# Performance work log

Hardware: AMD Instinct MI355X
Metric: run time of the kernel (lower is better)

The kernel has to match this reference:

```python
import jax, jax.numpy as jnp
import numpy as np

B, N, E, F, H, L = 64, 1024, 32768, 128, 32, 2
K = N // 2          # topk ratio 0.5 (fixed in source forward)
NB = 5              # num_neighbors: point cloud points per node
CF, P = 5, 50       # PI channels (filtration methods), PI_dim
OUT = 2

def gcn_conv(x, src, dst, emask, W, b, n):
    # PyG GCNConv: project first, symmetric norm with self-loops; emask zeroes filtered edges
    h = x @ W
    deg = jax.ops.segment_sum(emask, dst, num_segments=n) + 1.0
    dinv = jax.lax.rsqrt(deg)
    coef = (dinv[src] * dinv[dst] * emask)[:, None]
    agg = jax.ops.segment_sum(h[src] * coef, dst, num_segments=n)
    return agg + h * (dinv * dinv)[:, None] + b

def tcl(t, A, Bf, C):
    # Tensor Contraction Layer: mode-1/2/3 factor contraction
    return jnp.einsum('bijk,pi,qj,rk->bpqr', t, A, Bf, C)

def mlp2(h, Wa, ba, Wb, bb):
    return jax.nn.relu(h @ Wa + ba) @ Wb + bb

def setup_inputs():
    key = jax.random.key(0)
    ks = jax.random.split(key, 32)
    s = 0.05
    return {
        'x1': jax.random.normal(ks[0], (B, N, F), jnp.float32),
        'edge_index1': jax.random.randint(ks[1], (B, 2, E), 0, N),
        'PI1': jax.random.uniform(ks[2], (B, CF, P, P), dtype=jnp.float32),
        'x2': jax.random.normal(ks[3], (B, N, F), jnp.float32),
        'edge_index2': jax.random.randint(ks[4], (B, 2, E), 0, N),
        'PI2': jax.random.uniform(ks[5], (B, CF, P, P), dtype=jnp.float32),
        'W_score': jax.random.normal(ks[6], (F, NB * 2)) * s,
        'b_score': jnp.zeros((NB * 2,)),
        'W_gcn0': jax.random.normal(ks[7], (F, H)) * s,
        'b_gcn0': jnp.zeros((H,)),
        'Wm0a': jax.random.normal(ks[8], (H, H)) * s,
        'bm0a': jnp.zeros((H,)),
        'Wm0b': jax.random.normal(ks[9], (H, H * H)) * s,
        'bm0b': jnp.zeros((H * H,)),
        'W_gcn1': jax.random.normal(ks[10], (H * H, H)) * s,
        'b_gcn1': jnp.zeros((H,)),
        'Wm1a': jax.random.normal(ks[11], (H, H)) * s,
        'bm1a': jnp.zeros((H,)),
        'Wm1b': jax.random.normal(ks[12], (H, H * H)) * s,
        'bm1b': jnp.zeros((H * H,)),
        'F0': jax.random.normal(ks[13], (H, L)) * s,
        'F1': jax.random.normal(ks[14], (H, H)) * s,
        'F2': jax.random.normal(ks[15], (H, H)) * s,
        'K_conv': jax.random.normal(ks[16], (H, CF, 2, 2)) * s,
        'b_conv': jnp.zeros((H,)),
        'G0': jax.random.normal(ks[17], (H, H)) * s,
        'G1': jax.random.normal(ks[18], (H, P // 2)) * s,
        'G2': jax.random.normal(ks[19], (H, P // 2)) * s,
        'H0': jax.random.normal(ks[20], (2 * H, 2 * H)) * s,
        'H1': jax.random.normal(ks[21], (H, H)) * s,
        'H2': jax.random.normal(ks[22], (H, H)) * s,
        'Wo1': jax.random.normal(ks[23], (H, H)) * s,
        'bo1': jnp.zeros((H,)),
        'Wo2': jax.random.normal(ks[24], (H, OUT)) * s,
        'bo2': jnp.zeros((OUT,)),
    }

def reference(x1, edge_index1, PI1, x2, edge_index2, PI2, W_score, b_score,
              W_gcn0, b_gcn0, Wm0a, bm0a, Wm0b, bm0b,
              W_gcn1, b_gcn1, Wm1a, bm1a, Wm1b, bm1b,
              F0, F1, F2, K_conv, b_conv, G0, G1, G2,
              H0, H1, H2, Wo1, bo1, Wo2, bo2):
    ones = jnp.ones((E,), jnp.float32)

    def pool_one(xg, s_, d_):
        # score_node_layer -> point cloud -> lifespan score -> topk(0.5) -> filter_adj
        emb = gcn_conv(xg, s_, d_, ones, W_score, b_score, N)
        pc = emb.reshape(N, NB, 2)
        score = jnp.abs(pc[..., 1] - pc[..., 0]).sum(-1)
        _, perm = jax.lax.top_k(score, K)
        newidx = jnp.full((N,), -1).at[perm].set(jnp.arange(K))
        r, c = newidx[s_], newidx[d_]
        valid = (r >= 0) & (c >= 0)
        return xg[perm], jnp.where(valid, r, 0), jnp.where(valid, c, 0), valid.astype(jnp.float32)

    def branch(x, ei, PI):
        src, dst = ei[:, 0, :], ei[:, 1, :]
        xp, psrc, pdst, em = jax.vmap(pool_one)(x, src, dst)
        conv0 = jax.vmap(lambda h, s_, d_, m: gcn_conv(h, s_, d_, m, W_gcn0, b_gcn0, K))
        conv1 = jax.vmap(lambda h, s_, d_, m: gcn_conv(h, s_, d_, m, W_gcn1, b_gcn1, K))
        h1 = mlp2(conv0(xp, psrc, pdst, em), Wm0a, bm0a, Wm0b, bm0b)   # [B,K,H*H]
        h2 = mlp2(conv1(h1, psrc, pdst, em), Wm1a, bm1a, Wm1b, bm1b)   # [B,K,H*H]
        g = jnp.stack([h1.mean(1), h2.mean(1)], axis=1).reshape(B, L, H, H)
        gcn_t = tcl(g, F0, F1, F2)                                      # [B,H,H,H]
        pe = jax.lax.conv_general_dilated(PI, K_conv, (2, 2), 'VALID',
                                          dimension_numbers=('NCHW', 'OIHW', 'NCHW'))
        pe = jax.nn.relu(pe + b_conv[None, :, None, None])              # [B,H,25,25]
        pi_t = tcl(pe, G0, G1, G2)                                      # [B,H,H,H]
        fused = tcl(jnp.concatenate([gcn_t, pi_t], axis=1), H0, H1, H2) # [B,2H,H,H]
        pooled = fused.mean(axis=(1, 3))                                # [B,H]
        return jax.nn.relu(pooled @ Wo1 + bo1) @ Wo2 + bo2              # [B,OUT]

    return jnp.stack([branch(x1, edge_index1, PI1), branch(x2, edge_index2, PI2)])
```

## Files before the change

### kernel.cpp

```cpp
#include <hip/hip_runtime.h>
#include <cstdint>


constexpr int B_ = 64, N_ = 1024, E_ = 32768, F_ = 128, H_ = 32;
constexpr int CF_ = 5, P_ = 50, K_ = 512, G_ = 128, PO = 25;

constexpr size_t WS_SRCS  = 0;
constexpr size_t WS_ONODE = WS_SRCS + (size_t)G_*(E_/2);
constexpr size_t WS_VDEG  = WS_ONODE + (size_t)G_*K_;
constexpr size_t WS_EOFF  = WS_VDEG + (size_t)G_*(K_/2);
constexpr size_t WS_DINV  = WS_EOFF + (size_t)G_*K_;
constexpr size_t WS_GA    = WS_DINV + (size_t)G_*K_;
constexpr size_t WS_GC    = WS_GA + (size_t)G_*K_*H_;
constexpr size_t WS_PM0   = WS_GC + (size_t)G_*K_*H_;
constexpr size_t WS_PM1   = WS_PM0 + (size_t)G_*64;
constexpr size_t WS_PPI   = WS_PM1 + (size_t)G_*64;
constexpr size_t WS_F0V   = WS_PPI + (size_t)G_*32;
constexpr size_t WS_B01   = WS_F0V + 32;
constexpr size_t WS_C0B   = WS_B01 + 32;
constexpr size_t WS_C1B   = WS_C0B + 32;
constexpr size_t WS_W01   = WS_C1B + 32;
constexpr size_t WS_P0B   = WS_W01 + 1024;
constexpr size_t WS_P1B   = WS_P0B + 1024;

constexpr size_t WS_DSC   = WS_GC;

static __device__ __forceinline__ int swzf4(int row, int c4) {
  return row*32 + (((c4) ^ ((row >> 2) & 7)) << 2);
}

__global__ __launch_bounds__(512, 4) void kA_pre(
    const float* __restrict__ x1, const float* __restrict__ x2,
    const float* __restrict__ Wsc,
    const float* __restrict__ F0w, const float* __restrict__ F2w,
    const float* __restrict__ H0w, const float* __restrict__ H2w,
    const float* __restrict__ Wm0b, const float* __restrict__ bm0b,
    const float* __restrict__ Wm1b, const float* __restrict__ bm1b,
    const float* __restrict__ Wg1, float* __restrict__ ws)
{
  __shared__ float SM[640];
  int blk = blockIdx.x, t = threadIdx.x;

  if (blk < 8*G_) {
    int g = blk >> 3, sub = blk & 7, br = g >> 6, b = g & 63;
    const float* xg = (br ? x2 : x1) + (size_t)b*N_*F_;
    float* WdL = SM;
    if (t < F_) {
      #pragma unroll
      for (int j = 0; j < 5; ++j) WdL[t*5+j] = Wsc[t*10+2*j+1] - Wsc[t*10+2*j];
    }
    __syncthreads();
    int row = sub*128 + (t >> 2), q = t & 3;
    const float4* xr = (const float4*)(xg + (size_t)row*F_);
    float acc[5] = {};
    #pragma unroll
    for (int i = 0; i < 8; ++i) {
      int k4 = q + 4*i;
      float4 v = xr[k4];
      const float* w = &WdL[k4*20];
      #pragma unroll
      for (int j = 0; j < 5; ++j)
        acc[j] += v.x*w[j] + v.y*w[5+j] + v.z*w[10+j] + v.w*w[15+j];
    }
    #pragma unroll
    for (int j = 0; j < 5; ++j) {
      acc[j] += __shfl_xor(acc[j], 1, 4);
      acc[j] += __shfl_xor(acc[j], 2, 4);
    }
    if (q == 0) {
      float* o = ws + WS_DSC + ((size_t)g*N_ + row)*5;
      #pragma unroll
      for (int j = 0; j < 5; ++j) o[j] = acc[j];
    }
    return;
  }

  int blk2 = blk - 8*G_;
  if (blk2 == 0) {
    float* h0mS = SM;
    if (t < 32) { float s = 0.f; for (int qq = 0; qq < 64; ++qq) s += H0w[qq*64+t]; h0mS[t] = s*(1.f/64.f); }
    __syncthreads();
    if (t < 2) { float s = 0.f; for (int p = 0; p < 32; ++p) s += F0w[p*2+t]*h0mS[p]; ws[WS_F0V+t] = s; }
  } else if (blk2 <= 32) {
    int kk = blk2 - 1;
    int ol = t >> 4, seg = t & 15;
    const float4* ar = (const float4*)(Wm0b + (size_t)kk*1024 + seg*64);
    float s = 0.f;
    #pragma unroll
    for (int i = 0; i < 16; ++i) {
      float4 a = ar[i];
      int tt = seg*64 + i*4;
      s += a.x*Wg1[(tt+0)*32 + ol] + a.y*Wg1[(tt+1)*32 + ol]
         + a.z*Wg1[(tt+2)*32 + ol] + a.w*Wg1[(tt+3)*32 + ol];
    }
    s += __shfl_xor(s, 1, 16);
    s += __shfl_xor(s, 2, 16);
    s += __shfl_xor(s, 4, 16);
    s += __shfl_xor(s, 8, 16);
    if (seg == 0) ws[WS_W01 + kk*32 + ol] = s;
  } else if (blk2 == 33) {
    float* red = SM;
    int j = t & 31, seg = t >> 5;
    float s = 0.f;
    #pragma unroll
    for (int i = 0; i < 64; ++i) {
      int k = seg*64 + i;
      s += bm0b[k]*Wg1[k*32 + j];
    }
    red[seg*32 + j] = s;
    __syncthreads();
    if (t < 32) {
      float a = 0.f;
      #pragma unroll
      for (int q = 0; q < 16; ++q) a += red[q*32 + t];
      ws[WS_B01 + t] = a;
    }
  } else {
    const float* Wb = (blk2 == 34) ? Wm0b : Wm1b;
    const float* bb = (blk2 == 34) ? bm0b : bm1b;
    size_t dstP = (blk2 == 34) ? WS_P0B : WS_P1B;
    size_t dstC = (blk2 == 34) ? WS_C0B : WS_C1B;
    float* h2mL = SM;
    float* f2vL = SM + 32;
    if (t < 32) { float s = 0.f; for (int r = 0; r < 32; ++r) s += H2w[r*32+t]; h2mL[t] = s*(1.f/32.f); }
    __syncthreads();
    if (t < 32) { float s = 0.f; for (int r = 0; r < 32; ++r) s += F2w[r*32+t]*h2mL[r]; f2vL[t] = s; }
    __syncthreads();
    if (t < 256) {
      #pragma unroll
      for (int q = 0; q < 4; ++q) {
        int e = t*4 + q;
        int k = e >> 5, c = e & 31;
        float s = 0.f;
        #pragma unroll
        for (int kp = 0; kp < 32; ++kp) s += Wb[k*1024 + c*32 + kp]*f2vL[kp];
        ws[dstP + e] = s;
      }
    }
    if (t < 32) {
      float s = 0.f;
      #pragma unroll
      for (int kp = 0; kp < 32; ++kp) s += bb[t*32+kp]*f2vL[kp];
      ws[dstC+t] = s;
    }
  }
}

__global__ __launch_bounds__(256, 4) void kPI(
    const float* __restrict__ PI1, const float* __restrict__ PI2,
    const float* __restrict__ Kc, const float* __restrict__ bc,
    const float* __restrict__ G0w, const float* __restrict__ G2w,
    const float* __restrict__ H0w, const float* __restrict__ H2w,
    float* __restrict__ ws)
{
  int g = blockIdx.x, br = g >> 6, b = g & 63;
  const float* pig = (br ? PI2 : PI1) + (size_t)b*CF_*P_*P_;
  __shared__ float PIt[CF_*P_*P_];
  __shared__ float KcL[H_*CF_*4];
  __shared__ float bcL[H_], g0L[H_], g2L[PO], h2L[H_], hhL[H_];
  __shared__ float scr[640];
  int t = threadIdx.x;
  for (int i = t; i < CF_*P_*P_; i += 256) PIt[i] = pig[i];
  for (int i = t; i < H_*CF_*4; i += 256) KcL[i] = Kc[i];
  {
    int p = t >> 3, s = t & 7;
    float v = 0.f;
    #pragma unroll
    for (int q = 0; q < 8; ++q) v += H0w[(s + q*8)*64 + 32 + p];
    #pragma unroll
    for (int d = 4; d > 0; d >>= 1) v += __shfl_down(v, d, 8);
    if (s == 0) hhL[p] = v * (1.f/64.f);
  }
  {
    int r = t >> 3, s = t & 7;
    float v = 0.f;
    #pragma unroll
    for (int q = 0; q < 4; ++q) v += H2w[(s + q*8)*32 + r];
    #pragma unroll
    for (int d = 4; d > 0; d >>= 1) v += __shfl_down(v, d, 8);
    if (s == 0) h2L[r] = v * (1.f/32.f);
  }
  if (t < 32) bcL[t] = bc[t];
  __syncthreads();
  if (t < 32) { float s = 0.f; for (int p = 0; p < 32; ++p) s += G0w[p*32+t]*hhL[p]; g0L[t] = s; }
  if (t >= 64 && t < 64+PO) {
    int kp = t - 64;
    float s = 0.f;
    for (int r = 0; r < 32; ++r) s += G2w[r*25+kp]*h2L[r];
    g2L[kp] = s;
  }
  __syncthreads();
  for (int pos = t; pos < PO*PO; pos += 256) {
    int jp = pos / PO, kp = pos - jp*PO;
    float p00[CF_], p01[CF_], p10[CF_], p11[CF_];
    #pragma unroll
    for (int c = 0; c < CF_; ++c) {
      const float* q = &PIt[c*2500 + (2*jp)*50 + 2*kp];
      p00[c] = q[0]; p01[c] = q[1]; p10[c] = q[50]; p11[c] = q[51];
    }
    float acc = 0.f;
    for (int i = 0; i < H_; ++i) {
      float v = bcL[i];
      const float* kcp = &KcL[i*20];
      #pragma unroll
      for (int c = 0; c < CF_; ++c)
        v += p00[c]*kcp[c*4+0] + p01[c]*kcp[c*4+1] + p10[c]*kcp[c*4+2] + p11[c]*kcp[c*4+3];
      acc += fmaxf(v, 0.f) * g0L[i];
    }
    scr[pos] = acc * g2L[kp];
  }
  __syncthreads();
  if (t < PO) {
    float s = 0.f;
    #pragma unroll
    for (int k = 0; k < PO; ++k) s += scr[t*PO + k];
    ws[WS_PPI + (size_t)g*32 + t] = s;
  }
}

__global__ __launch_bounds__(1024, 4) void kBS(
    const int* __restrict__ ei1, const int* __restrict__ ei2,
    const float* __restrict__ bsc, float* __restrict__ ws)
{
  int g = blockIdx.x, br = g >> 6, b = g & 63;
  const int* ei  = (br ? ei2 : ei1) + (size_t)b*2*E_;
  const int* src = ei;
  const int* dst = ei + E_;
  int* onodeg = (int*)ws + WS_ONODE + (size_t)g*K_;
  uint16_t* vdegg = (uint16_t*)(ws + WS_VDEG) + (size_t)g*K_;
  int* ceoffg = (int*)ws + WS_EOFF + (size_t)g*K_;
  float* dinvg = ws + WS_DINV + (size_t)g*K_;
  uint16_t* csrc = (uint16_t*)(ws + WS_SRCS) + (size_t)g*E_;

  __shared__ uint16_t srcL[E_];
  __shared__ float DscL[N_*5];
  __shared__ float dinvF[N_];
  __shared__ int fbL[N_];
  __shared__ int fillL[N_];
  __shared__ int nidxL[N_];
  __shared__ int seoffL[K_];
  __shared__ int vdegL[K_];
  __shared__ int ceoffL[K_];
  __shared__ int hist[256], hsum[256];
  __shared__ int wtot[16], wbase[16], wsum[16];
  __shared__ int remL, dstarL;

  int t = threadIdx.x;
  { const float* Dg = ws + WS_DSC + (size_t)g*N_*5;
    for (int i = t; i < N_*5; i += 1024) DscL[i] = Dg[i]; }
  fillL[t] = 0;
  if (t < 256) hist[t] = 0;
  if (t == 0) remL = K_;
  __syncthreads();

  uint32_t ep[32];
  #pragma unroll
  for (int i = 0; i < 32; ++i) {
    int e = t + i*1024;
    int s = src[e], d = dst[e];
    ep[i] = (uint32_t)s | ((uint32_t)d << 16);
    atomicAdd(&fillL[d], 1);
  }
  __syncthreads();

  int c = fillL[t];
  int lane = t & 63, w = t >> 6;
  int x = c;
  #pragma unroll
  for (int s = 1; s < 64; s <<= 1) {
    int v = __shfl_up(x, s);
    if (lane >= s) x += v;
  }
  if (lane == 63) wsum[w] = x;
  __syncthreads();
  if (w == 0 && lane < 16) {
    int y = wsum[lane];
    #pragma unroll
    for (int s = 1; s < 16; s <<= 1) {
      int v = __shfl_up(y, s, 16);
      if (lane >= s) y += v;
    }
    wsum[lane] = y;
  }
  __syncthreads();
  int off0 = ((w == 0) ? 0 : wsum[w-1]) + x - c;
  int off1 = off0 + c;
  fbL[t] = off0;
  dinvF[t] = rsqrtf((float)c + 1.0f);
  fillL[t] = 0;
  __syncthreads();

  #pragma unroll
  for (int i = 0; i < 32; ++i) {
    int d = (int)(ep[i] >> 16), s = (int)(ep[i] & 0xffffu);
    int pos = fbL[d] + atomicAdd(&fillL[d], 1);
    srcL[pos] = (uint16_t)s;
  }
  __syncthreads();

  uint32_t key;
  {
    float agg[5] = {};
    for (int e = off0; e < off1; ++e) {
      int s = srcL[e];
      float dvs = dinvF[s];
      const float* hr = &DscL[s*5];
      #pragma unroll
      for (int j = 0; j < 5; ++j) agg[j] += hr[j]*dvs;
    }
    float dv = dinvF[t];
    const float* hn = &DscL[t*5];
    float sc = 0.f;
    #pragma unroll
    for (int j = 0; j < 5; ++j)
      sc += fabsf(dv*(agg[j] + dv*hn[j]) + (bsc[2*j+1] - bsc[2*j]));
    key = __float_as_uint(sc);
  }
  __syncthreads();

  uint32_t pref = 0, prefMask = 0;
  #pragma unroll
  for (int pass = 0; pass < 4; ++pass) {
    int shift = 24 - 8*pass;
    bool cand = (key & prefMask) == pref;
    if (cand) atomicAdd(&hist[(key >> shift) & 255], 1);
    __syncthreads();
    if (w == 0) {
      int base = lane*4;
      int h0 = hist[base+0], h1 = hist[base+1], h2 = hist[base+2], h3 = hist[base+3];
      int suf = h0 + h1 + h2 + h3;
      #pragma unroll
      for (int sh = 1; sh < 64; sh <<= 1) {
        int v = __shfl_down(suf, sh);
        if (lane + sh < 64) suf += v;
      }
      hsum[base+0] = suf;
      hsum[base+1] = suf - h0;
      hsum[base+2] = suf - h0 - h1;
      hsum[base+3] = suf - h0 - h1 - h2;
    }
    __syncthreads();
    int rem = remL;
    if (t < 256) {
      int above = (t == 255) ? 0 : hsum[t+1];
      if (hsum[t] >= rem && above < rem) dstarL = t;
      hist[t] = 0;
    }
    __syncthreads();
    int ds = dstarL;
    if (t == 0) remL = rem - ((ds == 255) ? 0 : hsum[ds+1]);
    pref |= (uint32_t)ds << shift;
    prefMask |= 0xFFu << shift;
  }
  __syncthreads();
  uint32_t T = pref;
  int r = remL;

  bool eq = (key == T);
  uint64_t mEq = __ballot(eq);
  int lpEq = (int)__popcll(mEq & ((1ull << lane) - 1));
  if (lane == 0) wtot[w] = (int)__popcll(mEq);
  __syncthreads();
  if (t == 0) { int a = 0; for (int q = 0; q < 16; ++q) { wbase[q] = a; a += wtot[q]; } }
  __syncthreads();
  bool sel = (key > T) || (eq && (wbase[w] + lpEq) < r);
  __syncthreads();
  uint64_t mS = __ballot(sel);
  int lpS = (int)__popcll(mS & ((1ull << lane) - 1));
  if (lane == 0) wtot[w] = (int)__popcll(mS);
  __syncthreads();
  if (t == 0) { int a = 0; for (int q = 0; q < 16; ++q) { wbase[q] = a; a += wtot[q]; } }
  __syncthreads();
  int rank = wbase[w] + lpS;
  nidxL[t] = sel ? rank : -1;
  if (sel) onodeg[rank] = t;
  __syncthreads();

  if (sel) {
    int c2 = 0;
    for (int e = off0; e < off1; ++e) {
      int m = nidxL[srcL[e]];
      if (m >= 0) srcL[off0 + (c2++)] = (uint16_t)m;
    }
    vdegL[rank] = c2;
    seoffL[rank] = off0;
  }
  __syncthreads();

  int vv = 0, xx = 0, w2 = t >> 6;
  if (t < K_) {
    vv = vdegL[t]; xx = vv;
    int l2 = t & 63;
    #pragma unroll
    for (int s = 1; s < 64; s <<= 1) {
      int v = __shfl_up(xx, s);
      if (l2 >= s) xx += v;
    }
    if (l2 == 63) wsum[w2] = xx;
  }
  __syncthreads();
  if (t == 0) { int run = 0; for (int q = 0; q < 8; ++q) { int tm = wsum[q]; wsum[q] = run; run += tm; } }
  __syncthreads();
  if (t < K_) {
    int ce = wsum[w2] + xx - vv;
    ceoffL[t] = ce;
    ceoffg[t] = ce;
    vdegg[t] = (uint16_t)vv;
    dinvg[t] = rsqrtf((float)vv + 1.0f);
  }
  __syncthreads();

  int tot = ceoffL[K_-1] + vdegL[K_-1];
  for (int p = t; p < tot; p += 1024) {
    int lo2 = 0, hi2 = K_ - 1;
    while (lo2 < hi2) {
      int mid = (lo2 + hi2 + 1) >> 1;
      if (ceoffL[mid] <= p) lo2 = mid; else hi2 = mid - 1;
    }
    csrc[p] = srcL[seoffL[lo2] + (p - ceoffL[lo2])];
  }
}

static __device__ __forceinline__ void mmA(
    const float* __restrict__ S, const float* __restrict__ Wp,
    float (&acc)[4][4], int it, int jt)
{
  const int i0 = it*4, swa = it & 7;
  #pragma unroll
  for (int kv = 0; kv < 8; ++kv) {
    float4 w0 = *(const float4*)&Wp[(kv*4+0)*36 + jt*4];
    float4 w1 = *(const float4*)&Wp[(kv*4+1)*36 + jt*4];
    float4 w2 = *(const float4*)&Wp[(kv*4+2)*36 + jt*4];
    float4 w3 = *(const float4*)&Wp[(kv*4+3)*36 + jt*4];
    #pragma unroll
    for (int d = 0; d < 4; ++d) {
      float4 a = *(const float4*)&S[(i0+d)*32 + ((kv ^ swa) << 2)];
      acc[d][0] += a.x*w0.x + a.y*w1.x + a.z*w2.x + a.w*w3.x;
      acc[d][1] += a.x*w0.y + a.y*w1.y + a.z*w2.y + a.w*w3.y;
      acc[d][2] += a.x*w0.z + a.y*w1.z + a.z*w2.z + a.w*w3.z;
      acc[d][3] += a.x*w0.w + a.y*w1.w + a.z*w2.w + a.w*w3.w;
    }
  }
}

__global__ __launch_bounds__(512, 4) void kG1(
    const float* __restrict__ x1, const float* __restrict__ x2,
    const float* __restrict__ Wg0, float* __restrict__ ws)
{
  int g = blockIdx.x, half = blockIdx.y, br = g >> 6, b = g & 63;
  const float* xg = (br ? x2 : x1) + (size_t)b*N_*F_;
  const int* onodeg = (const int*)ws + WS_ONODE + (size_t)g*K_ + half*256;
  const float* dinvg = ws + WS_DINV + (size_t)g*K_ + half*256;
  float* gAg = ws + WS_GA + (size_t)g*K_*H_ + (size_t)half*256*H_;

  __shared__ float wbuf[F_*36];
  __shared__ int   onodeL[256];
  __shared__ float dinvL[256];

  int t = threadIdx.x;
  for (int i = t; i < F_*H_; i += 512) wbuf[(i >> 5)*36 + (i & 31)] = Wg0[i];
  if (t < 256) { onodeL[t] = onodeg[t]; dinvL[t] = dinvg[t]; }
  __syncthreads();

  const int it = t >> 3, jt = t & 7;
  const int i0 = it*4;
  const float* xr0 = xg + (size_t)onodeL[i0+0]*F_;
  const float* xr1 = xg + (size_t)onodeL[i0+1]*F_;
  const float* xr2 = xg + (size_t)onodeL[i0+2]*F_;
  const float* xr3 = xg + (size_t)onodeL[i0+3]*F_;
  float acc[4][4] = {};
  for (int k4 = 0; k4 < 32; ++k4) {
    float4 w0 = *(const float4*)&wbuf[(k4*4+0)*36 + jt*4];
    float4 w1 = *(const float4*)&wbuf[(k4*4+1)*36 + jt*4];
    float4 w2 = *(const float4*)&wbuf[(k4*4+2)*36 + jt*4];
    float4 w3 = *(const float4*)&wbuf[(k4*4+3)*36 + jt*4];
    float4 a;
    a = *(const float4*)(xr0 + k4*4);
    acc[0][0]+=a.x*w0.x+a.y*w1.x+a.z*w2.x+a.w*w3.x; acc[0][1]+=a.x*w0.y+a.y*w1.y+a.z*w2.y+a.w*w3.y;
    acc[0][2]+=a.x*w0.z+a.y*w1.z+a.z*w2.z+a.w*w3.z; acc[0][3]+=a.x*w0.w+a.y*w1.w+a.z*w2.w+a.w*w3.w;
    a = *(const float4*)(xr1 + k4*4);
    acc[1][0]+=a.x*w0.x+a.y*w1.x+a.z*w2.x+a.w*w3.x; acc[1][1]+=a.x*w0.y+a.y*w1.y+a.z*w2.y+a.w*w3.y;
    acc[1][2]+=a.x*w0.z+a.y*w1.z+a.z*w2.z+a.w*w3.z; acc[1][3]+=a.x*w0.w+a.y*w1.w+a.z*w2.w+a.w*w3.w;
    a = *(const float4*)(xr2 + k4*4);
    acc[2][0]+=a.x*w0.x+a.y*w1.x+a.z*w2.x+a.w*w3.x; acc[2][1]+=a.x*w0.y+a.y*w1.y+a.z*w2.y+a.w*w3.y;
    acc[2][2]+=a.x*w0.z+a.y*w1.z+a.z*w2.z+a.w*w3.z; acc[2][3]+=a.x*w0.w+a.y*w1.w+a.z*w2.w+a.w*w3.w;
    a = *(const float4*)(xr3 + k4*4);
    acc[3][0]+=a.x*w0.x+a.y*w1.x+a.z*w2.x+a.w*w3.x; acc[3][1]+=a.x*w0.y+a.y*w1.y+a.z*w2.y+a.w*w3.y;
    acc[3][2]+=a.x*w0.z+a.y*w1.z+a.z*w2.z+a.w*w3.z; acc[3][3]+=a.x*w0.w+a.y*w1.w+a.z*w2.w+a.w*w3.w;
  }
  #pragma unroll
  for (int d = 0; d < 4; ++d) {
    int row = i0 + d;
    float rs = dinvL[row];
    float4 o; o.x=acc[d][0]*rs; o.y=acc[d][1]*rs; o.z=acc[d][2]*rs; o.w=acc[d][3]*rs;
    *(float4*)&gAg[row*32 + jt*4] = o;
  }
}

static __device__ __forceinline__ void convG(
    const float* __restrict__ gS, float* __restrict__ cbuf,
    const float* __restrict__ bias, const float* __restrict__ dinvL,
    const int* __restrict__ eoffL, const int* __restrict__ vcntL,
    const uint16_t* __restrict__ srcS, int half, int t)
{
  int ddl = t & 255, hc = t >> 8;
  int dd = half*256 + ddl;
  int lo = eoffL[ddl], n = vcntL[ddl];
  int c0 = hc*16;
  float4 a0 = {0,0,0,0}, a1 = a0, a2 = a0, a3 = a0;
  for (int i = 0; i < n; ++i) {
    int ss = srcS[lo + i];
    const float* r = gS + ss*32 + c0;
    float4 v;
    v = *(const float4*)(r+0);  a0.x+=v.x; a0.y+=v.y; a0.z+=v.z; a0.w+=v.w;
    v = *(const float4*)(r+4);  a1.x+=v.x; a1.y+=v.y; a1.z+=v.z; a1.w+=v.w;
    v = *(const float4*)(r+8);  a2.x+=v.x; a2.y+=v.y; a2.z+=v.z; a2.w+=v.w;
    v = *(const float4*)(r+12); a3.x+=v.x; a3.y+=v.y; a3.z+=v.z; a3.w+=v.w;
  }
  { const float* r = gS + dd*32 + c0;
    float4 v;
    v = *(const float4*)(r+0);  a0.x+=v.x; a0.y+=v.y; a0.z+=v.z; a0.w+=v.w;
    v = *(const float4*)(r+4);  a1.x+=v.x; a1.y+=v.y; a1.z+=v.z; a1.w+=v.w;
    v = *(const float4*)(r+8);  a2.x+=v.x; a2.y+=v.y; a2.z+=v.z; a2.w+=v.w;
    v = *(const float4*)(r+12); a3.x+=v.x; a3.y+=v.y; a3.z+=v.z; a3.w+=v.w; }
  float dvd = dinvL[ddl];
  float4 r0, r1, r2, r3;
  r0.x = dvd*a0.x + bias[c0+0];  r0.y = dvd*a0.y + bias[c0+1];
  r0.z = dvd*a0.z + bias[c0+2];  r0.w = dvd*a0.w + bias[c0+3];
  r1.x = dvd*a1.x + bias[c0+4];  r1.y = dvd*a1.y + bias[c0+5];
  r1.z = dvd*a1.z + bias[c0+6];  r1.w = dvd*a1.w + bias[c0+7];
  r2.x = dvd*a2.x + bias[c0+8];  r2.y = dvd*a2.y + bias[c0+9];
  r2.z = dvd*a2.z + bias[c0+10]; r2.w = dvd*a2.w + bias[c0+11];
  r3.x = dvd*a3.x + bias[c0+12]; r3.y = dvd*a3.y + bias[c0+13];
  r3.z = dvd*a3.z + bias[c0+14]; r3.w = dvd*a3.w + bias[c0+15];
  int g4 = hc*4;
  *(float4*)&cbuf[swzf4(ddl, g4+0)] = r0;
  *(float4*)&cbuf[swzf4(ddl, g4+1)] = r1;
  *(float4*)&cbuf[swzf4(ddl, g4+2)] = r2;
  *(float4*)&cbuf[swzf4(ddl, g4+3)] = r3;
}

__global__ __launch_bounds__(512, 4) void kG2(
    const float* __restrict__ bg0,
    const float* __restrict__ Wm0a, const float* __restrict__ bm0a,
    float* __restrict__ ws)
{
  int g = blockIdx.x, half = blockIdx.y;
  const float* gAg = ws + WS_GA + (size_t)g*K_*H_;
  float* gCg = ws + WS_GC + (size_t)g*K_*H_;
  const uint16_t* srcS = (const uint16_t*)(ws + WS_SRCS) + (size_t)g*E_;
  const int* eoffg = (const int*)ws + WS_EOFF + (size_t)g*K_ + half*256;
  const uint16_t* vdegg = (const uint16_t*)(ws + WS_VDEG) + (size_t)g*K_ + half*256;
  const float* dinvg = ws + WS_DINV + (size_t)g*K_ + half*256;

  __shared__ float cbufA[256*32];
  __shared__ float cbufB[256*32];
  __shared__ float wA[32*36];
  __shared__ float wB[32*36];
  __shared__ float scrP[64*33];
  __shared__ int   eoffL[256];
  __shared__ int   vcntL[256];
  __shared__ float dinvL[256];

  int t = threadIdx.x;
  for (int i = t; i < 1024; i += 512) {
    int k = i >> 5, j = i & 31;
    wA[k*36+j] = Wm0a[i];
    wB[k*36+j] = ws[WS_W01 + i];
  }
  if (t < 256) { eoffL[t] = eoffg[t]; vcntL[t] = vdegg[t]; dinvL[t] = dinvg[t]; }
  __syncthreads();

  convG(gAg, cbufA, bg0, dinvL, eoffL, vcntL, srcS, half, t);
  __syncthreads();

  const int it = t >> 3, jt = t & 7;
  float acc[4][4] = {};
  mmA(cbufA, wA, acc, it, jt);
  {
    float b0 = bm0a[jt*4+0], b1 = bm0a[jt*4+1], b2 = bm0a[jt*4+2], b3 = bm0a[jt*4+3];
    float cp0=0.f, cp1=0.f, cp2=0.f, cp3=0.f;
    #pragma unroll
    for (int d = 0; d < 4; ++d) {
      float v0=fmaxf(acc[d][0]+b0,0.f), v1=fmaxf(acc[d][1]+b1,0.f);
      float v2=fmaxf(acc[d][2]+b2,0.f), v3=fmaxf(acc[d][3]+b3,0.f);
      cp0+=v0; cp1+=v1; cp2+=v2; cp3+=v3;
      float4 o; o.x=v0; o.y=v1; o.z=v2; o.w=v3;
      *(float4*)&cbufB[swzf4(it*4+d, jt)] = o;
    }
    scrP[it*33 + jt*4+0] = cp0; scrP[it*33 + jt*4+1] = cp1;
    scrP[it*33 + jt*4+2] = cp2; scrP[it*33 + jt*4+3] = cp3;
  }
  __syncthreads();

  if (t < 32) {
    float s = 0.f;
    #pragma unroll
    for (int q = 0; q < 64; ++q) s += scrP[q*33 + t];
    ws[WS_PM0 + (size_t)g*64 + half*32 + t] = s;
  }

  float acc2[4][4] = {};
  mmA(cbufB, wB, acc2, it, jt);
  {
    float b0 = ws[WS_B01+jt*4+0], b1 = ws[WS_B01+jt*4+1];
    float b2 = ws[WS_B01+jt*4+2], b3 = ws[WS_B01+jt*4+3];
    #pragma unroll
    for (int d = 0; d < 4; ++d) {
      int row = it*4 + d;
      float rs = dinvL[row];
      float4 o;
      o.x=(acc2[d][0]+b0)*rs; o.y=(acc2[d][1]+b1)*rs;
      o.z=(acc2[d][2]+b2)*rs; o.w=(acc2[d][3]+b3)*rs;
      *(float4*)&gCg[(half*256+row)*32 + jt*4] = o;
    }
  }
}

__global__ __launch_bounds__(512, 4) void kG4(
    const float* __restrict__ bg1,
    const float* __restrict__ Wm1a, const float* __restrict__ bm1a,
    float* __restrict__ ws)
{
  int g = blockIdx.x, half = blockIdx.y;
  const float* gCg = ws + WS_GC + (size_t)g*K_*H_;
  const uint16_t* srcS = (const uint16_t*)(ws + WS_SRCS) + (size_t)g*E_;
  const int* eoffg = (const int*)ws + WS_EOFF + (size_t)g*K_ + half*256;
  const uint16_t* vdegg = (const uint16_t*)(ws + WS_VDEG) + (size_t)g*K_ + half*256;
  const float* dinvg = ws + WS_DINV + (size_t)g*K_ + half*256;

  __shared__ float cbufA[256*32];
  __shared__ float wA[32*36];
  __shared__ float scrP[64*33];
  __shared__ int   eoffL[256];
  __shared__ int   vcntL[256];
  __shared__ float dinvL[256];

  int t = threadIdx.x;
  for (int i = t; i < 1024; i += 512) wA[(i>>5)*36 + (i&31)] = Wm1a[i];
  if (t < 256) { eoffL[t] = eoffg[t]; vcntL[t] = vdegg[t]; dinvL[t] = dinvg[t]; }
  __syncthreads();

  convG(gCg, cbufA, bg1, dinvL, eoffL, vcntL, srcS, half, t);
  __syncthreads();

  const int it = t >> 3, jt = t & 7;
  float acc[4][4] = {};
  mmA(cbufA, wA, acc, it, jt);
  {
    float b0 = bm1a[jt*4+0], b1 = bm1a[jt*4+1], b2 = bm1a[jt*4+2], b3 = bm1a[jt*4+3];
    float cp0=0.f, cp1=0.f, cp2=0.f, cp3=0.f;
    #pragma unroll
    for (int d = 0; d < 4; ++d) {
      cp0 += fmaxf(acc[d][0]+b0,0.f); cp1 += fmaxf(acc[d][1]+b1,0.f);
      cp2 += fmaxf(acc[d][2]+b2,0.f); cp3 += fmaxf(acc[d][3]+b3,0.f);
    }
    scrP[it*33 + jt*4+0] = cp0; scrP[it*33 + jt*4+1] = cp1;
    scrP[it*33 + jt*4+2] = cp2; scrP[it*33 + jt*4+3] = cp3;
  }
  __syncthreads();

  if (t < 32) {
    float s = 0.f;
    #pragma unroll
    for (int q = 0; q < 64; ++q) s += scrP[q*33 + t];
    ws[WS_PM1 + (size_t)g*64 + half*32 + t] = s;
  }
}

__global__ __launch_bounds__(64) void k5_final(
    const float* __restrict__ F1w, const float* __restrict__ G1w,
    const float* __restrict__ H1w, const float* __restrict__ Wo1,
    const float* __restrict__ bo1, const float* __restrict__ Wo2,
    const float* __restrict__ bo2, const float* __restrict__ ws,
    float* __restrict__ out)
{
  int g = blockIdx.x, t = threadIdx.x;
  __shared__ float mr0[32], mr1[32], AL[32], TL[32], pl[32], zl[32], ppiL[PO];
  if (t < 32) {
    mr0[t] = (ws[WS_PM0 + (size_t)g*64 + t] + ws[WS_PM0 + (size_t)g*64 + 32 + t]) * (1.f/512.f);
    mr1[t] = (ws[WS_PM1 + (size_t)g*64 + t] + ws[WS_PM1 + (size_t)g*64 + 32 + t]) * (1.f/512.f);
  }
  if (t >= 32 && t < 32+PO) ppiL[t-32] = ws[WS_PPI + (size_t)g*32 + (t-32)];
  __syncthreads();
  float f00 = ws[WS_F0V], f01 = ws[WS_F0V+1];
  if (t < 32) {
    float s0 = ws[WS_C0B + t], s1 = ws[WS_C1B + t];
    for (int k = 0; k < 32; ++k) {
      s0 += mr0[k]*ws[WS_P0B + k*32 + t];
      s1 += mr1[k]*ws[WS_P1B + k*32 + t];
    }
    AL[t] = f00*s0 + f01*s1;
  }
  __syncthreads();
  if (t < 32) {
    float s = 0.f;
    for (int jp = 0; jp < 32; ++jp) s += F1w[t*32+jp]*AL[jp];
    for (int jp = 0; jp < PO; ++jp) s += G1w[t*25+jp]*ppiL[jp];
    TL[t] = s;
  }
  __syncthreads();
  if (t < 32) {
    float s = 0.f;
    for (int j = 0; j < 32; ++j) s += H1w[t*32+j]*TL[j];
    pl[t] = s;
  }
  __syncthreads();
  if (t < 32) {
    float s = bo1[t];
    for (int j = 0; j < 32; ++j) s += pl[j]*Wo1[j*32+t];
    zl[t] = fmaxf(s, 0.f);
  }
  __syncthreads();
  if (t < 2) {
    float s = bo2[t];
    for (int q = 0; q < 32; ++q) s += zl[q]*Wo2[q*2+t];
    int br = g >> 6, b = g & 63;
    out[br*(B_*2) + b*2 + t] = s;
  }
}

extern "C" void kernel_launch(void* const* d_in, const int* in_sizes, int n_in,
                              void* d_out, int out_size, void* d_ws, size_t ws_size,
                              hipStream_t stream) {
  (void)in_sizes; (void)n_in; (void)out_size; (void)ws_size;
  const float* x1      = (const float*)d_in[0];
  const int*   ei1     = (const int*)  d_in[1];
  const float* PI1     = (const float*)d_in[2];
  const float* x2      = (const float*)d_in[3];
  const int*   ei2     = (const int*)  d_in[4];
  const float* PI2     = (const float*)d_in[5];
  const float* W_score = (const float*)d_in[6];
  const float* b_score = (const float*)d_in[7];
  const float* W_gcn0  = (const float*)d_in[8];
  const float* b_gcn0  = (const float*)d_in[9];
  const float* Wm0a    = (const float*)d_in[10];
  const float* bm0a    = (const float*)d_in[11];
  const float* Wm0b    = (const float*)d_in[12];
  const float* bm0b    = (const float*)d_in[13];
  const float* W_gcn1  = (const float*)d_in[14];
  const float* b_gcn1  = (const float*)d_in[15];
  const float* Wm1a    = (const float*)d_in[16];
  const float* bm1a    = (const float*)d_in[17];
  const float* Wm1b    = (const float*)d_in[18];
  const float* bm1b    = (const float*)d_in[19];
  const float* F0w     = (const float*)d_in[20];
  const float* F1w     = (const float*)d_in[21];
  const float* F2w     = (const float*)d_in[22];
  const float* Kc      = (const float*)d_in[23];
  const float* bc      = (const float*)d_in[24];
  const float* G0w     = (const float*)d_in[25];
  const float* G1w     = (const float*)d_in[26];
  const float* G2w     = (const float*)d_in[27];
  const float* H0w     = (const float*)d_in[28];
  const float* H1w     = (const float*)d_in[29];
  const float* H2w     = (const float*)d_in[30];
  const float* Wo1     = (const float*)d_in[31];
  const float* bo1     = (const float*)d_in[32];
  const float* Wo2     = (const float*)d_in[33];
  const float* bo2     = (const float*)d_in[34];
  float* ws  = (float*)d_ws;
  float* out = (float*)d_out;

  kA_pre<<<8*G_ + 36, 512, 0, stream>>>(x1, x2, W_score,
                                        F0w, F2w, H0w, H2w,
                                        Wm0b, bm0b, Wm1b, bm1b, W_gcn1, ws);
  kPI<<<G_, 256, 0, stream>>>(PI1, PI2, Kc, bc, G0w, G2w, H0w, H2w, ws);
  kBS<<<G_, 1024, 0, stream>>>(ei1, ei2, b_score, ws);
  kG1<<<dim3(G_, 2), 512, 0, stream>>>(x1, x2, W_gcn0, ws);
  kG2<<<dim3(G_, 2), 512, 0, stream>>>(b_gcn0, Wm0a, bm0a, ws);
  kG4<<<dim3(G_, 2), 512, 0, stream>>>(b_gcn1, Wm1a, bm1a, ws);
  k5_final<<<G_, 64, 0, stream>>>(F1w, G1w, H1w, Wo1, bo1, Wo2, bo2, ws, out);
}
```

Measured before the change: 169.4 us.

## Merge PI conv kernel into edge-bucketing kernel and reuse first-pass atomic slots

```diff
diff --git a/kernel.cpp b/kernel.cpp
--- a/kernel.cpp
+++ b/kernel.cpp
@@ -146,92 +146,15 @@
   }
 }
 
-__global__ __launch_bounds__(256, 4) void kPI(
+__global__ __launch_bounds__(1024, 4) void kBSP(
+    const int* __restrict__ ei1, const int* __restrict__ ei2,
+    const float* __restrict__ bsc,
     const float* __restrict__ PI1, const float* __restrict__ PI2,
     const float* __restrict__ Kc, const float* __restrict__ bc,
     const float* __restrict__ G0w, const float* __restrict__ G2w,
     const float* __restrict__ H0w, const float* __restrict__ H2w,
     float* __restrict__ ws)
 {
-  int g = blockIdx.x, br = g >> 6, b = g & 63;
-  const float* pig = (br ? PI2 : PI1) + (size_t)b*CF_*P_*P_;
-  __shared__ float PIt[CF_*P_*P_];
-  __shared__ float KcL[H_*CF_*4];
-  __shared__ float bcL[H_], g0L[H_], g2L[PO], h2L[H_], hhL[H_];
-  __shared__ float scr[640];
-  int t = threadIdx.x;
-  for (int i = t; i < CF_*P_*P_; i += 256) PIt[i] = pig[i];
-  for (int i = t; i < H_*CF_*4; i += 256) KcL[i] = Kc[i];
-  {
-    int p = t >> 3, s = t & 7;
-    float v = 0.f;
-    #pragma unroll
-    for (int q = 0; q < 8; ++q) v += H0w[(s + q*8)*64 + 32 + p];
-    #pragma unroll
-    for (int d = 4; d > 0; d >>= 1) v += __shfl_down(v, d, 8);
-    if (s == 0) hhL[p] = v * (1.f/64.f);
-  }
-  {
-    int r = t >> 3, s = t & 7;
-    float v = 0.f;
-    #pragma unroll
-    for (int q = 0; q < 4; ++q) v += H2w[(s + q*8)*32 + r];
-    #pragma unroll
-    for (int d = 4; d > 0; d >>= 1) v += __shfl_down(v, d, 8);
-    if (s == 0) h2L[r] = v * (1.f/32.f);
-  }
-  if (t < 32) bcL[t] = bc[t];
-  __syncthreads();
-  if (t < 32) { float s = 0.f; for (int p = 0; p < 32; ++p) s += G0w[p*32+t]*hhL[p]; g0L[t] = s; }
-  if (t >= 64 && t < 64+PO) {
-    int kp = t - 64;
-    float s = 0.f;
-    for (int r = 0; r < 32; ++r) s += G2w[r*25+kp]*h2L[r];
-    g2L[kp] = s;
-  }
-  __syncthreads();
-  for (int pos = t; pos < PO*PO; pos += 256) {
-    int jp = pos / PO, kp = pos - jp*PO;
-    float p00[CF_], p01[CF_], p10[CF_], p11[CF_];
-    #pragma unroll
-    for (int c = 0; c < CF_; ++c) {
-      const float* q = &PIt[c*2500 + (2*jp)*50 + 2*kp];
-      p00[c] = q[0]; p01[c] = q[1]; p10[c] = q[50]; p11[c] = q[51];
-    }
-    float acc = 0.f;
-    for (int i = 0; i < H_; ++i) {
-      float v = bcL[i];
-      const float* kcp = &KcL[i*20];
-      #pragma unroll
-      for (int c = 0; c < CF_; ++c)
-        v += p00[c]*kcp[c*4+0] + p01[c]*kcp[c*4+1] + p10[c]*kcp[c*4+2] + p11[c]*kcp[c*4+3];
-      acc += fmaxf(v, 0.f) * g0L[i];
-    }
-    scr[pos] = acc * g2L[kp];
-  }
-  __syncthreads();
-  if (t < PO) {
-    float s = 0.f;
-    #pragma unroll
-    for (int k = 0; k < PO; ++k) s += scr[t*PO + k];
-    ws[WS_PPI + (size_t)g*32 + t] = s;
-  }
-}
-
-__global__ __launch_bounds__(1024, 4) void kBS(
-    const int* __restrict__ ei1, const int* __restrict__ ei2,
-    const float* __restrict__ bsc, float* __restrict__ ws)
-{
-  int g = blockIdx.x, br = g >> 6, b = g & 63;
-  const int* ei  = (br ? ei2 : ei1) + (size_t)b*2*E_;
-  const int* src = ei;
-  const int* dst = ei + E_;
-  int* onodeg = (int*)ws + WS_ONODE + (size_t)g*K_;
-  uint16_t* vdegg = (uint16_t*)(ws + WS_VDEG) + (size_t)g*K_;
-  int* ceoffg = (int*)ws + WS_EOFF + (size_t)g*K_;
-  float* dinvg = ws + WS_DINV + (size_t)g*K_;
-  uint16_t* csrc = (uint16_t*)(ws + WS_SRCS) + (size_t)g*E_;
-
   __shared__ uint16_t srcL[E_];
   __shared__ float DscL[N_*5];
   __shared__ float dinvF[N_];
@@ -245,7 +168,90 @@
   __shared__ int wtot[16], wbase[16], wsum[16];
   __shared__ int remL, dstarL;
 
-  int t = threadIdx.x;
+  int blk = blockIdx.x, t = threadIdx.x;
+
+  if (blk >= G_) {
+    int g = blk - G_, br = g >> 6, b = g & 63;
+    const float* pig = (br ? PI2 : PI1) + (size_t)b*CF_*P_*P_;
+    float* PIt = (float*)srcL;
+    float* KcL = DscL;
+    float* bcL = dinvF;
+    float* g0L = dinvF + 32;
+    float* g2L = dinvF + 64;
+    float* h2L = dinvF + 96;
+    float* hhL = dinvF + 128;
+    float* scr = (float*)fbL;
+
+    for (int i = t; i < CF_*P_*P_; i += 1024) PIt[i] = pig[i];
+    if (t < H_*CF_*4) KcL[t] = Kc[t];
+    if (t < 256) {
+      int p = t >> 3, s = t & 7;
+      float v = 0.f;
+      #pragma unroll
+      for (int q = 0; q < 8; ++q) v += H0w[(s + q*8)*64 + 32 + p];
+      #pragma unroll
+      for (int d = 4; d > 0; d >>= 1) v += __shfl_down(v, d, 8);
+      if (s == 0) hhL[p] = v * (1.f/64.f);
+    }
+    if (t >= 256 && t < 512) {
+      int tt = t - 256;
+      int r = tt >> 3, s = tt & 7;
+      float v = 0.f;
+      #pragma unroll
+      for (int q = 0; q < 4; ++q) v += H2w[(s + q*8)*32 + r];
+      #pragma unroll
+      for (int d = 4; d > 0; d >>= 1) v += __shfl_down(v, d, 8);
+      if (s == 0) h2L[r] = v * (1.f/32.f);
+    }
+    if (t >= 512 && t < 544) bcL[t - 512] = bc[t - 512];
+    __syncthreads();
+    if (t < 32) { float s = 0.f; for (int p = 0; p < 32; ++p) s += G0w[p*32+t]*hhL[p]; g0L[t] = s; }
+    if (t >= 64 && t < 64+PO) {
+      int kp = t - 64;
+      float s = 0.f;
+      for (int r = 0; r < 32; ++r) s += G2w[r*25+kp]*h2L[r];
+      g2L[kp] = s;
+    }
+    __syncthreads();
+    if (t < PO*PO) {
+      int jp = t / PO, kp = t - jp*PO;
+      float p00[CF_], p01[CF_], p10[CF_], p11[CF_];
+      #pragma unroll
+      for (int c = 0; c < CF_; ++c) {
+        const float* q = &PIt[c*2500 + (2*jp)*50 + 2*kp];
+        p00[c] = q[0]; p01[c] = q[1]; p10[c] = q[50]; p11[c] = q[51];
+      }
+      float acc = 0.f;
+      for (int i = 0; i < H_; ++i) {
+        float v = bcL[i];
+        const float* kcp = &KcL[i*20];
+        #pragma unroll
+        for (int c = 0; c < CF_; ++c)
+          v += p00[c]*kcp[c*4+0] + p01[c]*kcp[c*4+1] + p10[c]*kcp[c*4+2] + p11[c]*kcp[c*4+3];
+        acc += fmaxf(v, 0.f) * g0L[i];
+      }
+      scr[t] = acc * g2L[kp];
+    }
+    __syncthreads();
+    if (t < PO) {
+      float s = 0.f;
+      #pragma unroll
+      for (int k = 0; k < PO; ++k) s += scr[t*PO + k];
+      ws[WS_PPI + (size_t)g*32 + t] = s;
+    }
+    return;
+  }
+
+  int g = blk, br = g >> 6, b = g & 63;
+  const int* ei  = (br ? ei2 : ei1) + (size_t)b*2*E_;
+  const int* src = ei;
+  const int* dst = ei + E_;
+  int* onodeg = (int*)ws + WS_ONODE + (size_t)g*K_;
+  uint16_t* vdegg = (uint16_t*)(ws + WS_VDEG) + (size_t)g*K_;
+  int* ceoffg = (int*)ws + WS_EOFF + (size_t)g*K_;
+  float* dinvg = ws + WS_DINV + (size_t)g*K_;
+  uint16_t* csrc = (uint16_t*)(ws + WS_SRCS) + (size_t)g*E_;
+
   { const float* Dg = ws + WS_DSC + (size_t)g*N_*5;
     for (int i = t; i < N_*5; i += 1024) DscL[i] = Dg[i]; }
   fillL[t] = 0;
@@ -258,8 +264,8 @@
   for (int i = 0; i < 32; ++i) {
     int e = t + i*1024;
     int s = src[e], d = dst[e];
-    ep[i] = (uint32_t)s | ((uint32_t)d << 16);
-    atomicAdd(&fillL[d], 1);
+    int slot = atomicAdd(&fillL[d], 1);
+    ep[i] = (uint32_t)s | ((uint32_t)d << 10) | ((uint32_t)slot << 20);
   }
   __syncthreads();
 
@@ -287,14 +293,13 @@
   int off1 = off0 + c;
   fbL[t] = off0;
   dinvF[t] = rsqrtf((float)c + 1.0f);
-  fillL[t] = 0;
   __syncthreads();
 
   #pragma unroll
   for (int i = 0; i < 32; ++i) {
-    int d = (int)(ep[i] >> 16), s = (int)(ep[i] & 0xffffu);
-    int pos = fbL[d] + atomicAdd(&fillL[d], 1);
-    srcL[pos] = (uint16_t)s;
+    uint32_t e = ep[i];
+    int s = (int)(e & 0x3FFu), d = (int)((e >> 10) & 0x3FFu), slot = (int)(e >> 20);
+    srcL[fbL[d] + slot] = (uint16_t)s;
   }
   __syncthreads();
 
@@ -765,8 +770,8 @@
   kA_pre<<<8*G_ + 36, 512, 0, stream>>>(x1, x2, W_score,
                                         F0w, F2w, H0w, H2w,
                                         Wm0b, bm0b, Wm1b, bm1b, W_gcn1, ws);
-  kPI<<<G_, 256, 0, stream>>>(PI1, PI2, Kc, bc, G0w, G2w, H0w, H2w, ws);
-  kBS<<<G_, 1024, 0, stream>>>(ei1, ei2, b_score, ws);
+  kBSP<<<2*G_, 1024, 0, stream>>>(ei1, ei2, b_score, PI1, PI2, Kc, bc,
+                                  G0w, G2w, H0w, H2w, ws);
   kG1<<<dim3(G_, 2), 512, 0, stream>>>(x1, x2, W_gcn0, ws);
   kG2<<<dim3(G_, 2), 512, 0, stream>>>(b_gcn0, Wm0a, bm0a, ws);
   kG4<<<dim3(G_, 2), 512, 0, stream>>>(b_gcn1, Wm1a, bm1a, ws);
```

New measurement: 154.8 us. 8.7% less time.
